# Optimization experiments

Measured on AMD Instinct MI355X. Metric: run time of the kernel, lower is better.

Reference implementation:

```python
import jax, jax.numpy as jnp
import numpy as np

MULTIRES = 6          # positional-encoding frequencies (get_embedder)
SKIP_LAYER = 4        # skip_in=(4,) in ImplicitNetwork
BETA = 100.0          # Softplus(beta=100)
INV_SQRT2 = float(1.0 / np.sqrt(2.0))
NUM_NETS = 64         # multi displacement networks (clusters)


def embed(x):
    """NeRF positional embedding: [x, sin(2^k x), cos(2^k x)] for k=0..MULTIRES-1.
    x: [N,3] -> [N, 3 + 3*2*MULTIRES] = [N,39]."""
    outs = [x]
    for i in range(MULTIRES):
        f = float(2.0 ** i)
        outs.append(jnp.sin(f * x))
        outs.append(jnp.cos(f * x))
    return jnp.concatenate(outs, axis=-1)


def softplus100(x):
    # numerically stable softplus with beta=100
    return jnp.logaddexp(0.0, BETA * x) / BETA


def _forward(points,
             iW0, ib0, iW1, ib1, iW2, ib2, iW3, ib3, iW4, ib4,
             iW5, ib5, iW6, ib6, iW7, ib7, iW8, ib8,
             dW0, db0, dW1, db1, dW2, db2, dW3, db3,
             mW0, mb0, mW1, mb1, mW2, mb2):
    N = points.shape[0]
    inp = embed(points)  # [N,39]

    # ---- ImplicitNetwork: 9 linears, softplus(beta=100), skip concat at l=4 ----
    iWs = [iW0, iW1, iW2, iW3, iW4, iW5, iW6, iW7, iW8]
    ibs = [ib0, ib1, ib2, ib3, ib4, ib5, ib6, ib7, ib8]
    x = inp
    for l in range(9):
        if l == SKIP_LAYER:
            x = jnp.concatenate([x, inp], axis=1) * INV_SQRT2  # [N,473+39=512]
        x = x @ iWs[l].T + ibs[l]
        if l < 8:
            x = softplus100(x)
    sdf_feat = x  # [N,257] = sdf (1) + feature vector (256)

    # ---- DisplacementNetwork: 4 linears, ReLU on hidden, Tanh output ----
    xd = inp
    for W, b, last in ((dW0, db0, False), (dW1, db1, False), (dW2, db2, False), (dW3, db3, True)):
        xd = xd @ W.T + b
        xd = jnp.tanh(xd) if last else jax.nn.relu(xd)
    disp = xd  # [N,3]

    # ---- MultiDisplacementNetwork: batched per-cluster MLPs via bmm ----
    xm = inp.reshape(NUM_NETS, -1, inp.shape[1])  # [n, N/n, 39]
    xm = jax.nn.relu(jnp.einsum('nbi,noi->nbo', xm, mW0) + mb0[:, None, :])
    xm = jax.nn.relu(jnp.einsum('nbi,noi->nbo', xm, mW1) + mb1[:, None, :])
    xm = jnp.tanh(jnp.einsum('nbi,noi->nbo', xm, mW2) + mb2[:, None, :])
    mdisp = xm.reshape(N, 3)

    return jnp.concatenate([sdf_feat, disp, mdisp], axis=1)  # [N, 263]


def setup_inputs() -> dict:
    key = jax.random.key(0)
    ks = iter(jax.random.split(key, 80))
    N = 32768
    d = {}
    d['points'] = jax.random.uniform(next(ks), (N, 3), jnp.float32, -1.0, 1.0)

    def mk(out, inn):
        W = jax.random.normal(next(ks), (out, inn), jnp.float32) * (1.0 / np.sqrt(inn))
        b = jax.random.normal(next(ks), (out,), jnp.float32) * 0.01
        return W, b

    impl_shapes = [(512, 39), (512, 512), (512, 512), (473, 512), (512, 512),
                   (512, 512), (512, 512), (512, 512), (257, 512)]
    for l, (o, i) in enumerate(impl_shapes):
        d[f'iW{l}'], d[f'ib{l}'] = mk(o, i)

    disp_shapes = [(512, 39), (512, 512), (512, 512), (3, 512)]
    for l, (o, i) in enumerate(disp_shapes):
        d[f'dW{l}'], d[f'db{l}'] = mk(o, i)

    multi_shapes = [(128, 39), (128, 128), (3, 128)]
    for l, (o, i) in enumerate(multi_shapes):
        W = jax.random.normal(next(ks), (NUM_NETS, o, i), jnp.float32) * (1.0 / np.sqrt(i))
        b = jax.random.normal(next(ks), (NUM_NETS, o), jnp.float32) * 0.01
        d[f'mW{l}'], d[f'mb{l}'] = W, b
    return d


def reference(points,
              iW0, ib0, iW1, ib1, iW2, ib2, iW3, ib3, iW4, ib4,
              iW5, ib5, iW6, ib6, iW7, ib7, iW8, ib8,
              dW0, db0, dW1, db1, dW2, db2, dW3, db3,
              mW0, mb0, mW1, mb1, mW2, mb2):
    return _forward(points,
                    iW0, ib0, iW1, ib1, iW2, ib2, iW3, ib3, iW4, ib4,
                    iW5, ib5, iW6, ib6, iW7, ib7, iW8, ib8,
                    dW0, db0, dW1, db1, dW2, db2, dW3, db3,
                    mW0, mb0, mW1, mb1, mW2, mb2)
```

## Files before the change

kernel.cpp:

```cpp
#include <hip/hip_runtime.h>
#include <hip/hip_bf16.h>
#include <stdint.h>

typedef __attribute__((ext_vector_type(8))) short short8;
typedef __attribute__((ext_vector_type(4))) float floatx4;
typedef __attribute__((ext_vector_type(2))) uint uint2v;

#define INV_SQRT2F 0.70710678118654752440f
#define ROWS 128
#define NT 1024

__device__ ushort g_wbuf[4259840];

__device__ __forceinline__ ushort f2bf(float f) {
    union { float f; uint32_t u; } c; c.f = f;
    uint32_t x = c.u;
    return (ushort)((x + 0x7fffu + ((x >> 16) & 1u)) >> 16);
}
__device__ __forceinline__ uint pk2bf(float a, float b) {
    union { __hip_bfloat162 h; uint u; } c;
    c.h = __float22bfloat162_rn(make_float2(a, b));
    return c.u;
}
__device__ __forceinline__ float softplus100(float x) {
    float z = 100.f * x;
    return fmaxf(x, 0.f) + __logf(1.f + __expf(-fabsf(z))) * 0.01f;
}
__device__ __forceinline__ void bar_lgkm() {
    asm volatile("s_waitcnt lgkmcnt(0)\n\ts_barrier" ::: "memory");
}
__device__ __forceinline__ int fidx(int K32, int row, int ch) {
    return (((row >> 4) * K32 + (ch >> 5)) * 64 + ((ch >> 3) & 3) * 16 + (row & 15)) * 8 + (ch & 7);
}

struct Seg { const float* s; int off, nout, kw, k32, ttot, nclust; };
struct CvtAll { Seg seg[16]; };

__global__ void k_cvt(CvtAll c) {
    Seg sg = c.seg[blockIdx.y];
    ushort* d = g_wbuf + sg.off;
    const int pcs8 = sg.ttot * sg.k32 * 64;
    const int tot8 = pcs8 * sg.nclust;
    const bool vec = ((sg.kw & 7) == 0);
    for (int i8 = blockIdx.x * blockDim.x + threadIdx.x; i8 < tot8;
         i8 += gridDim.x * blockDim.x) {
        int cl = i8 / pcs8;
        int r = i8 - cl * pcs8;
        int t = r / (sg.k32 * 64);
        int r2 = r - t * (sg.k32 * 64);
        int kc = r2 >> 6;
        int lane = r2 & 63;
        int n = t * 16 + (lane & 15);
        int kb = kc * 32 + (lane >> 4) * 8;
        const float* src = sg.s + (size_t)cl * sg.nout * sg.kw;
        short8 v = {0, 0, 0, 0, 0, 0, 0, 0};
        if (n < sg.nout) {
            if (vec && kb + 8 <= sg.kw) {
                const float4* s4 = (const float4*)(src + (size_t)n * sg.kw + kb);
                float4 a = s4[0], b = s4[1];
                v[0] = (short)f2bf(a.x); v[1] = (short)f2bf(a.y);
                v[2] = (short)f2bf(a.z); v[3] = (short)f2bf(a.w);
                v[4] = (short)f2bf(b.x); v[5] = (short)f2bf(b.y);
                v[6] = (short)f2bf(b.z); v[7] = (short)f2bf(b.w);
            } else {
#pragma unroll
                for (int j = 0; j < 8; ++j) {
                    int k = kb + j;
                    if (k < sg.kw) v[j] = (short)f2bf(src[(size_t)n * sg.kw + k]);
                }
            }
        }
        *(short8*)(d + (size_t)i8 * 8) = v;
    }
}

template<int K32OUT>
__device__ void embedR(short* act, const float* pts, int row0, short* inp_sv) {
    for (int idx = threadIdx.x; idx < ROWS * 64; idx += NT) {
        int row = idx >> 6, col = idx & 63;
        float v = 0.f;
        if (col < 39) {
            int comp = (col < 3) ? col : (col - 3) % 3;
            float x = pts[(row0 + row) * 3 + comp];
            if (col < 3) v = x;
            else {
                int b = col - 3; int fi = b / 6; int r = b % 6;
                float a = x * (float)(1 << fi);
                v = (r < 3) ? __sinf(a) : __cosf(a);
            }
        }
        act[fidx(K32OUT, row, col)] = (short)f2bf(v);
        if (inp_sv && col < 39) inp_sv[row * 40 + col] = (short)f2bf(v * INV_SQRT2F);
    }
}

template<int ACT, int K32IN, int K32OUT, bool FULL>
__device__ void layer_mm(short* act, const ushort* __restrict__ Wf,
                         short8 (&pre)[2],
                         const ushort* __restrict__ Wfn, int k32n, int Ttn,
                         const float* __restrict__ bias, int Nout, float scale,
                         bool toLds, float* gOut, int gCol0, int gRow0)
{
    const int tid = threadIdx.x;
    const int wave = tid >> 6, lane = tid & 63;
    const int q = lane >> 4, li = lane & 15;
    const int lane8 = lane * 8;
    const int Ttot = FULL ? 32 : ((Nout + 15) >> 4);

    floatx4 acc[2][8];
#pragma unroll
    for (int i = 0; i < 2; ++i)
#pragma unroll
        for (int m = 0; m < 8; ++m) acc[i][m] = (floatx4){0.f, 0.f, 0.f, 0.f};

    bool tv[2]; const ushort* wb[2];
#pragma unroll
    for (int i = 0; i < 2; ++i) {
        int t = wave + 16 * i;
        tv[i] = FULL ? true : (t < Ttot);
        wb[i] = Wf + (size_t)t * K32IN * 512 + lane8;
    }

    if (FULL || tv[0]) {
        auto loadB = [&](int kc, short8* b) {
#pragma unroll
            for (int i = 0; i < 2; ++i)
                if (FULL || tv[i]) b[i] = *(const short8*)(wb[i] + kc * 512);
        };
        auto step = [&](int kc, short8* b) {
#pragma unroll
            for (int h = 0; h < 2; ++h) {
                short8 afr[4];
#pragma unroll
                for (int m2 = 0; m2 < 4; ++m2)
                    afr[m2] = *(const short8*)&act[((h * 4 + m2) * K32IN + kc) * 512 + lane8];
                __builtin_amdgcn_s_setprio(1);
#pragma unroll
                for (int i = 0; i < 2; ++i) {
                    if (!(FULL || tv[i])) continue;
#pragma unroll
                    for (int m2 = 0; m2 < 4; ++m2)
                        acc[i][h * 4 + m2] = __builtin_amdgcn_mfma_f32_16x16x32_bf16(
                            b[i], afr[m2], acc[i][h * 4 + m2], 0, 0, 0);
                }
                __builtin_amdgcn_s_setprio(0);
            }
        };

        short8 b0[2], b1[2];
#pragma unroll
        for (int i = 0; i < 2; ++i) b0[i] = pre[i];
#pragma unroll
        for (int kc = 0; kc < K32IN; kc += 2) {
            if (kc + 1 < K32IN) loadB(kc + 1, b1);
            step(kc, b0);
            if (kc + 2 < K32IN) loadB(kc + 2, b0);
            if (kc + 1 < K32IN) step(kc + 1, b1);
        }
    }
    if (Wfn) {
#pragma unroll
        for (int i = 0; i < 2; ++i) {
            int t = wave + 16 * i;
            if (t < Ttn)
                pre[i] = *(const short8*)(Wfn + (size_t)t * k32n * 512 + lane8);
        }
    }
    bar_lgkm();
#pragma unroll
    for (int i = 0; i < 2; ++i) {
        if (!(FULL || tv[i])) continue;
        const int nb = (wave + 16 * i) * 16 + q * 4;
        if (!FULL && nb >= Nout) continue;
        const bool fullN = FULL || (nb + 4) <= Nout;
        float bs[4];
        if (fullN) {
            float4 b4 = *(const float4*)(bias + nb);
            bs[0] = b4.x; bs[1] = b4.y; bs[2] = b4.z; bs[3] = b4.w;
        } else {
#pragma unroll
            for (int r = 0; r < 4; ++r) bs[r] = (nb + r < Nout) ? bias[nb + r] : 0.f;
        }
        const int wbase = ((nb >> 5)) * 512 + ((nb >> 3) & 3) * 128 + li * 8 + (nb & 7);
#pragma unroll
        for (int m = 0; m < 8; ++m) {
            const int row = m * 16 + li;
            float v[4];
#pragma unroll
            for (int r = 0; r < 4; ++r) {
                float x = acc[i][m][r] + bs[r];
                if (ACT == 1) x = softplus100(x);
                else if (ACT == 2) x = fmaxf(x, 0.f);
                else if (ACT == 3) x = tanhf(x);
                v[r] = x * scale;
            }
            if (toLds) {
                if (fullN) {
                    uint2v pk = {pk2bf(v[0], v[1]), pk2bf(v[2], v[3])};
                    *(uint2v*)&act[m * K32OUT * 512 + wbase] = pk;
                } else {
#pragma unroll
                    for (int r = 0; r < 4; ++r)
                        if (nb + r < Nout)
                            act[fidx(K32OUT, row, nb + r)] = (short)f2bf(v[r]);
                }
            } else {
#pragma unroll
                for (int r = 0; r < 4; ++r)
                    if (nb + r < Nout)
                        gOut[(size_t)(gRow0 + row) * 263 + gCol0 + nb + r] = v[r];
            }
        }
    }
}

struct IP { int iw[9]; const float* ib[9]; };
struct DMP { int dw[4]; const float* db[4]; int mw[3]; const float* mb[3]; };
struct AllP { IP ip; DMP dm; };

struct LayerCtx {
    short* act; short* inp_sv; const float* pts; float* out; int row0;
};

__device__ void run_impl(LayerCtx& c, const IP& p, short8 (&pre)[2],
                         const ushort* nextW, int nextK32, int nextT) {
    embedR<2>(c.act, c.pts, c.row0, c.inp_sv);
    bar_lgkm();
    layer_mm<1, 2, 16, true>(c.act, g_wbuf + p.iw[0], pre, g_wbuf + p.iw[1], 16, 32,
                             p.ib[0], 512, 1.f, true, nullptr, 0, 0);
    bar_lgkm();
    layer_mm<1, 16, 16, true>(c.act, g_wbuf + p.iw[1], pre, g_wbuf + p.iw[2], 16, 32,
                              p.ib[1], 512, 1.f, true, nullptr, 0, 0);
    bar_lgkm();
    layer_mm<1, 16, 16, true>(c.act, g_wbuf + p.iw[2], pre, g_wbuf + p.iw[3], 16, 30,
                              p.ib[2], 512, 1.f, true, nullptr, 0, 0);
    bar_lgkm();
    layer_mm<1, 16, 16, false>(c.act, g_wbuf + p.iw[3], pre, g_wbuf + p.iw[4], 16, 32,
                               p.ib[3], 473, INV_SQRT2F, true, nullptr, 0, 0);
    for (int t2 = threadIdx.x; t2 < ROWS * 64; t2 += NT) {
        int row = t2 >> 6, col = t2 & 63;
        if (col < 39) c.act[fidx(16, row, 473 + col)] = c.inp_sv[row * 40 + col];
    }
    bar_lgkm();
    layer_mm<1, 16, 16, true>(c.act, g_wbuf + p.iw[4], pre, g_wbuf + p.iw[5], 16, 32,
                              p.ib[4], 512, 1.f, true, nullptr, 0, 0);
    bar_lgkm();
    layer_mm<1, 16, 16, true>(c.act, g_wbuf + p.iw[5], pre, g_wbuf + p.iw[6], 16, 32,
                              p.ib[5], 512, 1.f, true, nullptr, 0, 0);
    bar_lgkm();
    layer_mm<1, 16, 16, true>(c.act, g_wbuf + p.iw[6], pre, g_wbuf + p.iw[7], 16, 32,
                              p.ib[6], 512, 1.f, true, nullptr, 0, 0);
    bar_lgkm();
    layer_mm<1, 16, 16, true>(c.act, g_wbuf + p.iw[7], pre, g_wbuf + p.iw[8], 16, 17,
                              p.ib[7], 512, 1.f, true, nullptr, 0, 0);
    bar_lgkm();
    layer_mm<0, 16, 16, false>(c.act, g_wbuf + p.iw[8], pre, nextW, nextK32, nextT,
                               p.ib[8], 257, 1.f, false, c.out, 0, c.row0);
}

__device__ void run_dm(LayerCtx& c, const DMP& p, int rpc, short8 (&pre)[2]) {
    const int cl = c.row0 / rpc;
    const ushort* w0 = g_wbuf + p.mw[0] + cl * 8192;
    const ushort* w1 = g_wbuf + p.mw[1] + cl * 16384;
    const ushort* w2 = g_wbuf + p.mw[2] + cl * 2048;
    embedR<2>(c.act, c.pts, c.row0, nullptr);
    bar_lgkm();
    layer_mm<2, 2, 4, false>(c.act, w0, pre, w1, 4, 8,
                             p.mb[0] + cl * 128, 128, 1.f, true, nullptr, 0, 0);
    bar_lgkm();
    layer_mm<2, 4, 4, false>(c.act, w1, pre, w2, 4, 1,
                             p.mb[1] + cl * 128, 128, 1.f, true, nullptr, 0, 0);
    bar_lgkm();
    layer_mm<3, 4, 4, false>(c.act, w2, pre, g_wbuf + p.dw[0], 2, 32,
                             p.mb[2] + cl * 3, 3, 1.f, false, c.out, 260, c.row0);
    embedR<2>(c.act, c.pts, c.row0, nullptr);
    bar_lgkm();
    layer_mm<2, 2, 16, true>(c.act, g_wbuf + p.dw[0], pre, g_wbuf + p.dw[1], 16, 32,
                             p.db[0], 512, 1.f, true, nullptr, 0, 0);
    bar_lgkm();
    layer_mm<2, 16, 16, true>(c.act, g_wbuf + p.dw[1], pre, g_wbuf + p.dw[2], 16, 32,
                              p.db[1], 512, 1.f, true, nullptr, 0, 0);
    bar_lgkm();
    layer_mm<2, 16, 16, true>(c.act, g_wbuf + p.dw[2], pre, g_wbuf + p.dw[3], 16, 1,
                              p.db[2], 512, 1.f, true, nullptr, 0, 0);
    bar_lgkm();
    layer_mm<3, 16, 16, false>(c.act, g_wbuf + p.dw[3], pre, nullptr, 16, 0,
                               p.db[3], 3, 1.f, false, c.out, 257, c.row0);
}

__global__ __launch_bounds__(NT, 4) void k_all(const float* __restrict__ pts,
                                               AllP P, float* __restrict__ out,
                                               int rpc) {
    __shared__ __align__(16) short act[ROWS * 512];
    __shared__ short inp_sv[ROWS * 40];
    const int wave = threadIdx.x >> 6;
    const int lane8 = (threadIdx.x & 63) * 8;
    const int swz = (blockIdx.x & 7) * 32 + (blockIdx.x >> 3);
    LayerCtx c{act, inp_sv, pts, out, swz * ROWS};
    short8 pre[2];
    const int cl = c.row0 / rpc;
#pragma unroll
    for (int i = 0; i < 2; ++i)
        pre[i] = *(const short8*)(g_wbuf + P.ip.iw[0] +
                                  (size_t)(wave + 16 * i) * 2 * 512 + lane8);
    run_impl(c, P.ip, pre, g_wbuf + P.dm.mw[0] + cl * 8192, 2, 8);
    run_dm(c, P.dm, rpc, pre);
}

extern "C" void kernel_launch(void* const* d_in, const int* in_sizes, int n_in,
                              void* d_out, int out_size, void* d_ws, size_t ws_size,
                              hipStream_t stream) {
    const float* pts = (const float*)d_in[0];
    float* out = (float*)d_out;
    const int N = in_sizes[0] / 3;
    const int rpc = N / 64;

    const int iN[9] = {512, 512, 512, 473, 512, 512, 512, 512, 257};
    const int iK[9] = {39, 512, 512, 512, 512, 512, 512, 512, 512};
    const int dN[4] = {512, 512, 512, 3};
    const int dK[4] = {39, 512, 512, 512};
    const int mN[3] = {128, 128, 3};
    const int mK[3] = {39, 128, 128};

    CvtAll cv; AllP P;
    int off = 0, seg = 0;
    auto add_seg = [&](const float* src, int nout, int kw, int nclust) -> int {
        int k32 = ((kw + 31) & ~31) / 32;
        int ttot = (nout + 15) >> 4;
        cv.seg[seg].s = src; cv.seg[seg].off = off;
        cv.seg[seg].nout = nout; cv.seg[seg].kw = kw;
        cv.seg[seg].k32 = k32; cv.seg[seg].ttot = ttot; cv.seg[seg].nclust = nclust;
        int my = off;
        off += ttot * k32 * 512 * nclust;
        ++seg;
        return my;
    };
    for (int l = 0; l < 9; ++l) {
        P.ip.iw[l] = add_seg((const float*)d_in[1 + 2 * l], iN[l], iK[l], 1);
        P.ip.ib[l] = (const float*)d_in[2 + 2 * l];
    }
    for (int l = 0; l < 4; ++l) {
        P.dm.dw[l] = add_seg((const float*)d_in[19 + 2 * l], dN[l], dK[l], 1);
        P.dm.db[l] = (const float*)d_in[20 + 2 * l];
    }
    for (int l = 0; l < 3; ++l) {
        P.dm.mw[l] = add_seg((const float*)d_in[27 + 2 * l], mN[l], mK[l], 64);
        P.dm.mb[l] = (const float*)d_in[28 + 2 * l];
    }

    k_cvt<<<dim3(256, 16), 256, 0, stream>>>(cv);
    k_all<<<N / ROWS, NT, 0, stream>>>(pts, P, out, rpc);
}
```

Measured before the change: 482.7 us.

## Retile per-wave MFMA work into 4x4 N/M tiles and drop cross-layer weight prefetch

```diff
diff --git a/kernel.cpp b/kernel.cpp
--- a/kernel.cpp
+++ b/kernel.cpp
@@ -96,27 +96,26 @@
 
 template<int ACT, int K32IN, int K32OUT, bool FULL>
 __device__ void layer_mm(short* act, const ushort* __restrict__ Wf,
-                         short8 (&pre)[2],
-                         const ushort* __restrict__ Wfn, int k32n, int Ttn,
                          const float* __restrict__ bias, int Nout, float scale,
                          bool toLds, float* gOut, int gCol0, int gRow0)
 {
     const int tid = threadIdx.x;
     const int wave = tid >> 6, lane = tid & 63;
+    const int wg = wave & 7, mg = wave >> 3;
     const int q = lane >> 4, li = lane & 15;
     const int lane8 = lane * 8;
     const int Ttot = FULL ? 32 : ((Nout + 15) >> 4);
 
-    floatx4 acc[2][8];
-#pragma unroll
-    for (int i = 0; i < 2; ++i)
-#pragma unroll
-        for (int m = 0; m < 8; ++m) acc[i][m] = (floatx4){0.f, 0.f, 0.f, 0.f};
-
-    bool tv[2]; const ushort* wb[2];
-#pragma unroll
-    for (int i = 0; i < 2; ++i) {
-        int t = wave + 16 * i;
+    floatx4 acc[4][4];
+#pragma unroll
+    for (int i = 0; i < 4; ++i)
+#pragma unroll
+        for (int m = 0; m < 4; ++m) acc[i][m] = (floatx4){0.f, 0.f, 0.f, 0.f};
+
+    bool tv[4]; const ushort* wb[4];
+#pragma unroll
+    for (int i = 0; i < 4; ++i) {
+        int t = wg * 4 + i;
         tv[i] = FULL ? true : (t < Ttot);
         wb[i] = Wf + (size_t)t * K32IN * 512 + lane8;
     }
@@ -124,32 +123,32 @@
     if (FULL || tv[0]) {
         auto loadB = [&](int kc, short8* b) {
 #pragma unroll
-            for (int i = 0; i < 2; ++i)
+            for (int i = 0; i < 4; ++i)
                 if (FULL || tv[i]) b[i] = *(const short8*)(wb[i] + kc * 512);
         };
         auto step = [&](int kc, short8* b) {
 #pragma unroll
             for (int h = 0; h < 2; ++h) {
-                short8 afr[4];
-#pragma unroll
-                for (int m2 = 0; m2 < 4; ++m2)
-                    afr[m2] = *(const short8*)&act[((h * 4 + m2) * K32IN + kc) * 512 + lane8];
+                short8 afr[2];
+#pragma unroll
+                for (int m2 = 0; m2 < 2; ++m2)
+                    afr[m2] = *(const short8*)
+                        &act[((mg * 4 + h * 2 + m2) * K32IN + kc) * 512 + lane8];
                 __builtin_amdgcn_s_setprio(1);
 #pragma unroll
-                for (int i = 0; i < 2; ++i) {
+                for (int i = 0; i < 4; ++i) {
                     if (!(FULL || tv[i])) continue;
 #pragma unroll
-                    for (int m2 = 0; m2 < 4; ++m2)
-                        acc[i][h * 4 + m2] = __builtin_amdgcn_mfma_f32_16x16x32_bf16(
-                            b[i], afr[m2], acc[i][h * 4 + m2], 0, 0, 0);
+                    for (int m2 = 0; m2 < 2; ++m2)
+                        acc[i][h * 2 + m2] = __builtin_amdgcn_mfma_f32_16x16x32_bf16(
+                            b[i], afr[m2], acc[i][h * 2 + m2], 0, 0, 0);
                 }
                 __builtin_amdgcn_s_setprio(0);
             }
         };
 
-        short8 b0[2], b1[2];
-#pragma unroll
-        for (int i = 0; i < 2; ++i) b0[i] = pre[i];
+        short8 b0[4], b1[4];
+        loadB(0, b0);
 #pragma unroll
         for (int kc = 0; kc < K32IN; kc += 2) {
             if (kc + 1 < K32IN) loadB(kc + 1, b1);
@@ -158,19 +157,11 @@
             if (kc + 1 < K32IN) step(kc + 1, b1);
         }
     }
-    if (Wfn) {
-#pragma unroll
-        for (int i = 0; i < 2; ++i) {
-            int t = wave + 16 * i;
-            if (t < Ttn)
-                pre[i] = *(const short8*)(Wfn + (size_t)t * k32n * 512 + lane8);
-        }
-    }
-    bar_lgkm();
-#pragma unroll
-    for (int i = 0; i < 2; ++i) {
+    bar_lgkm();
+#pragma unroll
+    for (int i = 0; i < 4; ++i) {
         if (!(FULL || tv[i])) continue;
-        const int nb = (wave + 16 * i) * 16 + q * 4;
+        const int nb = (wg * 4 + i) * 16 + q * 4;
         if (!FULL && nb >= Nout) continue;
         const bool fullN = FULL || (nb + 4) <= Nout;
         float bs[4];
@@ -183,12 +174,13 @@
         }
         const int wbase = ((nb >> 5)) * 512 + ((nb >> 3) & 3) * 128 + li * 8 + (nb & 7);
 #pragma unroll
-        for (int m = 0; m < 8; ++m) {
-            const int row = m * 16 + li;
+        for (int m2 = 0; m2 < 4; ++m2) {
+            const int mAbs = mg * 4 + m2;
+            const int row = mAbs * 16 + li;
             float v[4];
 #pragma unroll
             for (int r = 0; r < 4; ++r) {
-                float x = acc[i][m][r] + bs[r];
+                float x = acc[i][m2][r] + bs[r];
                 if (ACT == 1) x = softplus100(x);
                 else if (ACT == 2) x = fmaxf(x, 0.f);
                 else if (ACT == 3) x = tanhf(x);
@@ -197,7 +189,7 @@
             if (toLds) {
                 if (fullN) {
                     uint2v pk = {pk2bf(v[0], v[1]), pk2bf(v[2], v[3])};
-                    *(uint2v*)&act[m * K32OUT * 512 + wbase] = pk;
+                    *(uint2v*)&act[mAbs * K32OUT * 512 + wbase] = pk;
                 } else {
 #pragma unroll
                     for (int r = 0; r < 4; ++r)
@@ -222,70 +214,53 @@
     short* act; short* inp_sv; const float* pts; float* out; int row0;
 };
 
-__device__ void run_impl(LayerCtx& c, const IP& p, short8 (&pre)[2],
-                         const ushort* nextW, int nextK32, int nextT) {
+__device__ void run_impl(LayerCtx& c, const IP& p) {
     embedR<2>(c.act, c.pts, c.row0, c.inp_sv);
     bar_lgkm();
-    layer_mm<1, 2, 16, true>(c.act, g_wbuf + p.iw[0], pre, g_wbuf + p.iw[1], 16, 32,
-                             p.ib[0], 512, 1.f, true, nullptr, 0, 0);
-    bar_lgkm();
-    layer_mm<1, 16, 16, true>(c.act, g_wbuf + p.iw[1], pre, g_wbuf + p.iw[2], 16, 32,
-                              p.ib[1], 512, 1.f, true, nullptr, 0, 0);
-    bar_lgkm();
-    layer_mm<1, 16, 16, true>(c.act, g_wbuf + p.iw[2], pre, g_wbuf + p.iw[3], 16, 30,
-                              p.ib[2], 512, 1.f, true, nullptr, 0, 0);
-    bar_lgkm();
-    layer_mm<1, 16, 16, false>(c.act, g_wbuf + p.iw[3], pre, g_wbuf + p.iw[4], 16, 32,
-                               p.ib[3], 473, INV_SQRT2F, true, nullptr, 0, 0);
+    layer_mm<1, 2, 16, true>(c.act, g_wbuf + p.iw[0], p.ib[0], 512, 1.f, true, nullptr, 0, 0);
+    bar_lgkm();
+    layer_mm<1, 16, 16, true>(c.act, g_wbuf + p.iw[1], p.ib[1], 512, 1.f, true, nullptr, 0, 0);
+    bar_lgkm();
+    layer_mm<1, 16, 16, true>(c.act, g_wbuf + p.iw[2], p.ib[2], 512, 1.f, true, nullptr, 0, 0);
+    bar_lgkm();
+    layer_mm<1, 16, 16, false>(c.act, g_wbuf + p.iw[3], p.ib[3], 473, INV_SQRT2F, true, nullptr, 0, 0);
     for (int t2 = threadIdx.x; t2 < ROWS * 64; t2 += NT) {
         int row = t2 >> 6, col = t2 & 63;
         if (col < 39) c.act[fidx(16, row, 473 + col)] = c.inp_sv[row * 40 + col];
     }
     bar_lgkm();
-    layer_mm<1, 16, 16, true>(c.act, g_wbuf + p.iw[4], pre, g_wbuf + p.iw[5], 16, 32,
-                              p.ib[4], 512, 1.f, true, nullptr, 0, 0);
-    bar_lgkm();
-    layer_mm<1, 16, 16, true>(c.act, g_wbuf + p.iw[5], pre, g_wbuf + p.iw[6], 16, 32,
-                              p.ib[5], 512, 1.f, true, nullptr, 0, 0);
-    bar_lgkm();
-    layer_mm<1, 16, 16, true>(c.act, g_wbuf + p.iw[6], pre, g_wbuf + p.iw[7], 16, 32,
-                              p.ib[6], 512, 1.f, true, nullptr, 0, 0);
-    bar_lgkm();
-    layer_mm<1, 16, 16, true>(c.act, g_wbuf + p.iw[7], pre, g_wbuf + p.iw[8], 16, 17,
-                              p.ib[7], 512, 1.f, true, nullptr, 0, 0);
-    bar_lgkm();
-    layer_mm<0, 16, 16, false>(c.act, g_wbuf + p.iw[8], pre, nextW, nextK32, nextT,
-                               p.ib[8], 257, 1.f, false, c.out, 0, c.row0);
-}
-
-__device__ void run_dm(LayerCtx& c, const DMP& p, int rpc, short8 (&pre)[2]) {
+    layer_mm<1, 16, 16, true>(c.act, g_wbuf + p.iw[4], p.ib[4], 512, 1.f, true, nullptr, 0, 0);
+    bar_lgkm();
+    layer_mm<1, 16, 16, true>(c.act, g_wbuf + p.iw[5], p.ib[5], 512, 1.f, true, nullptr, 0, 0);
+    bar_lgkm();
+    layer_mm<1, 16, 16, true>(c.act, g_wbuf + p.iw[6], p.ib[6], 512, 1.f, true, nullptr, 0, 0);
+    bar_lgkm();
+    layer_mm<1, 16, 16, true>(c.act, g_wbuf + p.iw[7], p.ib[7], 512, 1.f, true, nullptr, 0, 0);
+    bar_lgkm();
+    layer_mm<0, 16, 16, false>(c.act, g_wbuf + p.iw[8], p.ib[8], 257, 1.f, false, c.out, 0, c.row0);
+}
+
+__device__ void run_dm(LayerCtx& c, const DMP& p, int rpc) {
     const int cl = c.row0 / rpc;
     const ushort* w0 = g_wbuf + p.mw[0] + cl * 8192;
     const ushort* w1 = g_wbuf + p.mw[1] + cl * 16384;
     const ushort* w2 = g_wbuf + p.mw[2] + cl * 2048;
     embedR<2>(c.act, c.pts, c.row0, nullptr);
     bar_lgkm();
-    layer_mm<2, 2, 4, false>(c.act, w0, pre, w1, 4, 8,
-                             p.mb[0] + cl * 128, 128, 1.f, true, nullptr, 0, 0);
-    bar_lgkm();
-    layer_mm<2, 4, 4, false>(c.act, w1, pre, w2, 4, 1,
-                             p.mb[1] + cl * 128, 128, 1.f, true, nullptr, 0, 0);
-    bar_lgkm();
-    layer_mm<3, 4, 4, false>(c.act, w2, pre, g_wbuf + p.dw[0], 2, 32,
-                             p.mb[2] + cl * 3, 3, 1.f, false, c.out, 260, c.row0);
+    layer_mm<2, 2, 4, false>(c.act, w0, p.mb[0] + cl * 128, 128, 1.f, true, nullptr, 0, 0);
+    bar_lgkm();
+    layer_mm<2, 4, 4, false>(c.act, w1, p.mb[1] + cl * 128, 128, 1.f, true, nullptr, 0, 0);
+    bar_lgkm();
+    layer_mm<3, 4, 4, false>(c.act, w2, p.mb[2] + cl * 3, 3, 1.f, false, c.out, 260, c.row0);
     embedR<2>(c.act, c.pts, c.row0, nullptr);
     bar_lgkm();
-    layer_mm<2, 2, 16, true>(c.act, g_wbuf + p.dw[0], pre, g_wbuf + p.dw[1], 16, 32,
-                             p.db[0], 512, 1.f, true, nullptr, 0, 0);
-    bar_lgkm();
-    layer_mm<2, 16, 16, true>(c.act, g_wbuf + p.dw[1], pre, g_wbuf + p.dw[2], 16, 32,
-                              p.db[1], 512, 1.f, true, nullptr, 0, 0);
-    bar_lgkm();
-    layer_mm<2, 16, 16, true>(c.act, g_wbuf + p.dw[2], pre, g_wbuf + p.dw[3], 16, 1,
-                              p.db[2], 512, 1.f, true, nullptr, 0, 0);
-    bar_lgkm();
-    layer_mm<3, 16, 16, false>(c.act, g_wbuf + p.dw[3], pre, nullptr, 16, 0,
-                               p.db[3], 3, 1.f, false, c.out, 257, c.row0);
+    layer_mm<2, 2, 16, true>(c.act, g_wbuf + p.dw[0], p.db[0], 512, 1.f, true, nullptr, 0, 0);
+    bar_lgkm();
+    layer_mm<2, 16, 16, true>(c.act, g_wbuf + p.dw[1], p.db[1], 512, 1.f, true, nullptr, 0, 0);
+    bar_lgkm();
+    layer_mm<2, 16, 16, true>(c.act, g_wbuf + p.dw[2], p.db[2], 512, 1.f, true, nullptr, 0, 0);
+    bar_lgkm();
+    layer_mm<3, 16, 16, false>(c.act, g_wbuf + p.dw[3], p.db[3], 3, 1.f, false, c.out, 257, c.row0);
 }
 
 __global__ __launch_bounds__(NT, 4) void k_all(const float* __restrict__ pts,
@@ -293,18 +268,10 @@
                                                int rpc) {
     __shared__ __align__(16) short act[ROWS * 512];
     __shared__ short inp_sv[ROWS * 40];
-    const int wave = threadIdx.x >> 6;
-    const int lane8 = (threadIdx.x & 63) * 8;
     const int swz = (blockIdx.x & 7) * 32 + (blockIdx.x >> 3);
     LayerCtx c{act, inp_sv, pts, out, swz * ROWS};
-    short8 pre[2];
-    const int cl = c.row0 / rpc;
-#pragma unroll
-    for (int i = 0; i < 2; ++i)
-        pre[i] = *(const short8*)(g_wbuf + P.ip.iw[0] +
-                                  (size_t)(wave + 16 * i) * 2 * 512 + lane8);
-    run_impl(c, P.ip, pre, g_wbuf + P.dm.mw[0] + cl * 8192, 2, 8);
-    run_dm(c, P.dm, rpc, pre);
+    run_impl(c, P.ip);
+    run_dm(c, P.dm, rpc);
 }
 
 extern "C" void kernel_launch(void* const* d_in, const int* in_sizes, int n_in,
```

Result: faster. 463.8 us (-3.9%).
